# Kernel optimization log

Hardware: AMD Instinct MI355X
Metric: run time of the kernel (lower is better)

Reference implementation:

```python
import jax, jax.numpy as jnp
import numpy as np

# H2RConfig constants
KERNEL = 3
MAX_ROUTES = 1000
STRIDE = 4.0
MIN_SIZE = 32.0
MAX_SIZE = 512.0
SCORE_POWER = 2.0
UNC_WEIGHT = 0.35


def setup_inputs() -> dict:
    key = jax.random.key(0)
    k1, k2, k3 = jax.random.split(key, 3)
    shape = (32, 1, 512, 512)  # [B, 1, H, W] heatmaps at stride 4
    return {
        "route_logits": jax.random.normal(k1, shape, jnp.float32),
        "scale_logits": jax.random.normal(k2, shape, jnp.float32),
        "uncertainty_logits": jax.random.normal(k3, shape, jnp.float32),
        "image_h": 2048,
        "image_w": 2048,
    }


def reference(route_logits, scale_logits, uncertainty_logits, image_h, image_w):
    # score map: sigmoid^power, modulated by uncertainty (use_route_uncertainty=True)
    score = jnp.power(jax.nn.sigmoid(route_logits), SCORE_POWER)
    score = score * (1.0 - UNC_WEIGHT * jax.nn.sigmoid(uncertainty_logits))

    # local-max NMS: 3x3 max pool, stride 1, SAME padding (torch pads with -inf)
    pooled = jax.lax.reduce_window(
        score, -jnp.inf, jax.lax.max,
        window_dimensions=(1, 1, KERNEL, KERNEL),
        window_strides=(1, 1, 1, 1),
        padding="SAME",
    )
    peak_mask = score == pooled
    filtered = jnp.where(peak_mask, score, -1.0)

    B = score.shape[0]
    Wd = score.shape[3]
    flat = filtered.reshape(B, -1)                 # [B, H*W]
    values, indices = jax.lax.top_k(flat, MAX_ROUTES)  # [B, K]
    valid = values > 0.0                            # torch drops these; we mask/pad

    ys = indices // Wd
    xs = indices % Wd
    cx = (xs.astype(jnp.float32) + 0.5) * STRIDE
    cy = (ys.astype(jnp.float32) + 0.5) * STRIDE

    # gather scale / uncertainty at peak locations
    sc = jnp.take_along_axis(scale_logits.reshape(B, -1), indices, axis=1)
    un = jax.nn.sigmoid(jnp.take_along_axis(uncertainty_logits.reshape(B, -1), indices, axis=1))

    side = MIN_SIZE + jax.nn.sigmoid(sc) * (MAX_SIZE - MIN_SIZE)
    side = side * (1.0 + 0.25 * un)
    half = side * 0.5

    iw = float(image_w)
    ih = float(image_h)
    x1 = jnp.clip(cx - half, 0.0, iw - 1.0)
    y1 = jnp.clip(cy - half, 0.0, ih - 1.0)
    x2 = jnp.clip(cx + half, 1.0, iw)
    y2 = jnp.clip(cy + half, 1.0, ih)

    bcol = jnp.broadcast_to(jnp.arange(B, dtype=jnp.float32)[:, None], values.shape)
    rois = jnp.stack([bcol, x1, y1, x2, y2], axis=-1)  # [B, K, 5]

    # padded (fixed-shape) equivalent of torch's variable-length concat
    rois = jnp.where(valid[..., None], rois, 0.0)
    scores = jnp.where(valid, values, 0.0)
    return rois, scores, valid
```

## Files before the change

kernel.cpp:

```cpp
#include <hip/hip_runtime.h>
#include <hip/hip_bf16.h>
#include <math.h>


#define B_   32
#define H_   512
#define W_   512
#define HW_  (H_ * W_)
#define K_   1000
#define ROWS_ 16
#define THR_  512
#define PBUF_ 2048
#define PCAP_ 32768
#define CAND_ 2048
#define NBUK_ 4096

__device__ __forceinline__ float np_expf(float x) {
#pragma clang fp contract(off)
    const float log2e = 1.44269504088896341f;
    float z = x * log2e;
    float m = rintf(z);
    float r = fmaf(m, -0.693359375f, x);
    r = fmaf(m, 2.12194440e-4f, r);
    float r2 = r * r;
    float p = fmaf(1.9875691500e-4f, r, 1.3981999507e-3f);
    p = fmaf(p, r, 8.3334519073e-3f);
    p = fmaf(p, r, 4.1665795894e-2f);
    p = fmaf(p, r, 1.6666665459e-1f);
    p = fmaf(p, r, 5.0000001201e-1f);
    p = fmaf(p, r2, r);
    p = p + 1.0f;
    int mi = (int)m;
    float sc = __int_as_float((127 + mi) << 23);
    return p * sc;
}

__device__ __forceinline__ float sigmoid_np(float x) {
#pragma clang fp contract(off)
    float e = np_expf(-x);
    float d = 1.0f + e;
    return 1.0f / d;
}

__device__ __forceinline__ float score_ref(float r, float u) {
#pragma clang fp contract(off)
    float s  = sigmoid_np(r);
    float s2 = s * s;
    float su = sigmoid_np(u);
    float t  = 0.35f * su;
    float m  = 1.0f - t;
    return s2 * m;
}

__device__ __forceinline__ float sigmoid_fast(float x) {
    return 1.0f / (1.0f + __expf(-x));
}

__global__ __launch_bounds__(THR_, 4) void fused_peak_kernel(
    const float* __restrict__ route, const float* __restrict__ unc,
    unsigned long long* __restrict__ plist, int* __restrict__ peak_cnt)
{
    __shared__ float sm[ROWS_ + 2][W_];
    __shared__ unsigned long long pbuf[PBUF_];
    __shared__ int lcnt, gbase;

    const int tid   = threadIdx.x;
    const int strip = blockIdx.x;
    const int b     = blockIdx.y;
    const int r0    = strip * ROWS_;
    if (tid == 0) lcnt = 0;

    const float4* rb4 = (const float4*)(route + (size_t)b * HW_);
    const float4* ub4 = (const float4*)(unc   + (size_t)b * HW_);

    float4 rv[5], uv[5];
    int lrow[5], c4[5]; bool ok[5], act[5];
    #pragma unroll
    for (int k = 0; k < 5; ++k) {
        int slot = tid + k * THR_;
        act[k]  = slot < (ROWS_ + 2) * 128;
        int row = slot >> 7;
        int gy  = r0 - 1 + row;
        lrow[k] = row; c4[k] = slot & 127;
        ok[k]   = (gy >= 0 && gy < H_);
        int cy  = gy < 0 ? 0 : (gy >= H_ ? H_ - 1 : gy);
        if (act[k]) {
            rv[k] = rb4[cy * 128 + c4[k]];
            uv[k] = ub4[cy * 128 + c4[k]];
        }
    }
    #pragma unroll
    for (int k = 0; k < 5; ++k) {
        if (!act[k]) continue;
        float4 s;
        s.x = score_ref(rv[k].x, uv[k].x);
        s.y = score_ref(rv[k].y, uv[k].y);
        s.z = score_ref(rv[k].z, uv[k].z);
        s.w = score_ref(rv[k].w, uv[k].w);
        if (!ok[k]) { s.x = -INFINITY; s.y = -INFINITY;
                      s.z = -INFINITY; s.w = -INFINITY; }
        *(float4*)&sm[lrow[k]][c4[k] * 4] = s;
    }
    __syncthreads();

    #pragma unroll
    for (int j = 0; j < 4; ++j) {
        int g  = tid + j * THR_;
        int ly = 1 + (g >> 7);
        int x0 = (g & 127) * 4;
        int gy = r0 + (ly - 1);
        float4 q0 = *(const float4*)&sm[ly - 1][x0];
        float4 q1 = *(const float4*)&sm[ly    ][x0];
        float4 q2 = *(const float4*)&sm[ly + 1][x0];
        bool hasL = (x0 > 0), hasR = (x0 + 4 < W_);
        float l0 = hasL ? sm[ly - 1][x0 - 1] : -INFINITY;
        float l1 = hasL ? sm[ly    ][x0 - 1] : -INFINITY;
        float l2 = hasL ? sm[ly + 1][x0 - 1] : -INFINITY;
        float e0 = hasR ? sm[ly - 1][x0 + 4] : -INFINITY;
        float e1 = hasR ? sm[ly    ][x0 + 4] : -INFINITY;
        float e2 = hasR ? sm[ly + 1][x0 + 4] : -INFINITY;
        float f_m1 = fmaxf(l0, fmaxf(l1, l2));
        float f_0  = fmaxf(q0.x, fmaxf(q1.x, q2.x));
        float f_1  = fmaxf(q0.y, fmaxf(q1.y, q2.y));
        float f_2  = fmaxf(q0.z, fmaxf(q1.z, q2.z));
        float f_3  = fmaxf(q0.w, fmaxf(q1.w, q2.w));
        float f_4  = fmaxf(e0, fmaxf(e1, e2));
        float tb0  = fmaxf(q0.x, q2.x);
        float tb1  = fmaxf(q0.y, q2.y);
        float tb2  = fmaxf(q0.z, q2.z);
        float tb3  = fmaxf(q0.w, q2.w);
        float vv[4] = { q1.x, q1.y, q1.z, q1.w };
        float mm[4];
        mm[0] = fmaxf(fmaxf(f_m1, f_1), tb0);
        mm[1] = fmaxf(fmaxf(f_0,  f_2), tb1);
        mm[2] = fmaxf(fmaxf(f_1,  f_3), tb2);
        mm[3] = fmaxf(fmaxf(f_2,  f_4), tb3);
        #pragma unroll
        for (int i = 0; i < 4; ++i) {
            if (vv[i] >= mm[i]) {
                unsigned int bits = __float_as_uint(vv[i]);
                unsigned int idx  = (unsigned int)(gy * W_ + x0 + i);
                int p = atomicAdd(&lcnt, 1);
                if (p < PBUF_)
                    pbuf[p] = ((unsigned long long)bits << 32)
                              | (0xFFFFFFFFu - idx);
            }
        }
    }
    __syncthreads();
    if (tid == 0) {
        int n = lcnt < PBUF_ ? lcnt : PBUF_;
        gbase = atomicAdd(&peak_cnt[b], n);
    }
    __syncthreads();
    int n = lcnt < PBUF_ ? lcnt : PBUF_;
    int base = gbase;
    for (int i = tid; i < n; i += THR_) {
        int dst = base + i;
        if (dst < PCAP_) plist[(size_t)b * PCAP_ + dst] = pbuf[i];
    }
}

__global__ __launch_bounds__(1024) void select_kernel(
    const float* __restrict__ scale, const float* __restrict__ unc,
    const unsigned long long* __restrict__ plist,
    const int* __restrict__ peak_cnt,
    const int* __restrict__ ih_p, const int* __restrict__ iw_p,
    float* __restrict__ out)
{
    __shared__ unsigned int h16[NBUK_ / 2];
    __shared__ unsigned long long cand[CAND_];
    __shared__ int sh_T, sh_T2, sh_ref, sh_n;

    const int b = blockIdx.x, tid = threadIdx.x;
    const int lane = tid & 63, wid = tid >> 6;
    if (tid == 0) { sh_T = 0; sh_T2 = 0; sh_ref = 0; sh_n = 0; }
    for (int i = tid; i < NBUK_ / 2; i += 1024) h16[i] = 0u;
    __syncthreads();

    int pc = peak_cnt[b]; if (pc > PCAP_) pc = PCAP_;
    const unsigned long long* pl = plist + (size_t)b * PCAP_;

    for (int i = tid; i < pc; i += 1024) {
        unsigned int bkt = ((unsigned int)(pl[i] >> 32)) >> 18;
        atomicAdd(&h16[bkt >> 1], 1u << ((bkt & 1) * 16));
    }
    __syncthreads();

    if (wid == 0) {
        int total = 0;
        for (int c = NBUK_ / 64 - 1; c >= 0; --c) {
            int bucket = c * 64 + lane;
            int cnt = (int)((h16[bucket >> 1] >> ((bucket & 1) * 16)) & 0xFFFFu);
            int s = cnt;
            #pragma unroll
            for (int off = 32; off > 0; off >>= 1) s += __shfl_down(s, off, 64);
            s = __shfl(s, 0, 64);
            if (total + s < K_) { total += s; continue; }
            int suf = cnt;
            #pragma unroll
            for (int off = 1; off < 64; off <<= 1) {
                int o = __shfl_down(suf, off, 64);
                suf += (lane + off < 64) ? o : 0;
            }
            bool cond = (total + suf) >= K_;
            unsigned long long mask = __ballot(cond);
            int ls = 63 - __builtin_clzll(mask);
            int sufs = __shfl(suf, ls, 64);
            int cnts = __shfl(cnt, ls, 64);
            if (lane == 0) {
                sh_T = c * 64 + ls;
                int A = total + sufs - cnts;
                sh_ref = (A + cnts > 1024) ? (0x40000000 | A) : 0;
            }
            break;
        }
    }
    __syncthreads();
    const unsigned int T = (unsigned int)sh_T;
    const int refflag = sh_ref;
    const int refined = (refflag >> 30) & 1;
    const int A = refflag & 0x3FFFFFFF;

    if (refined) {
        for (int i = tid; i < NBUK_ / 2; i += 1024) h16[i] = 0u;
        __syncthreads();
        for (int i = tid; i < pc; i += 1024) {
            unsigned int bits = (unsigned int)(pl[i] >> 32);
            if ((bits >> 18) == T) {
                unsigned int sb = (bits >> 6) & 0xFFFu;
                atomicAdd(&h16[sb >> 1], 1u << ((sb & 1) * 16));
            }
        }
        __syncthreads();
        if (wid == 0) {
            int total = A;
            for (int c = NBUK_ / 64 - 1; c >= 0; --c) {
                int bucket = c * 64 + lane;
                int cnt = (int)((h16[bucket >> 1] >> ((bucket & 1) * 16)) & 0xFFFFu);
                int s = cnt;
                #pragma unroll
                for (int off = 32; off > 0; off >>= 1) s += __shfl_down(s, off, 64);
                s = __shfl(s, 0, 64);
                if (total + s < K_) { total += s; continue; }
                int suf = cnt;
                #pragma unroll
                for (int off = 1; off < 64; off <<= 1) {
                    int o = __shfl_down(suf, off, 64);
                    suf += (lane + off < 64) ? o : 0;
                }
                bool cond = (total + suf) >= K_;
                unsigned long long mask = __ballot(cond);
                int ls = 63 - __builtin_clzll(mask);
                if (lane == 0) sh_T2 = c * 64 + ls;
                break;
            }
        }
        __syncthreads();
    }
    const unsigned int T2 = (unsigned int)sh_T2;

    for (int i = tid; i < pc; i += 1024) {
        unsigned long long key = pl[i];
        unsigned int bits = (unsigned int)(key >> 32);
        unsigned int bkt  = bits >> 18;
        bool take = (bkt > T) ||
                    (bkt == T && (!refined || (((bits >> 6) & 0xFFFu) >= T2)));
        if (take) {
            int p = atomicAdd(&sh_n, 1);
            if (p < CAND_) cand[p] = key;
        }
    }
    __syncthreads();
    int nc = sh_n; if (nc > CAND_) nc = CAND_;
    int sortN = (nc <= 1024) ? 1024 : CAND_;
    for (int i = tid; i < sortN; i += 1024)
        if (i >= nc) cand[i] = 0ull;

    for (int kk = 2; kk <= sortN; kk <<= 1) {
        for (int jj = kk >> 1; jj > 0; jj >>= 1) {
            __syncthreads();
            for (int p = tid; p < (sortN >> 1); p += 1024) {
                int i   = ((p & ~(jj - 1)) << 1) | (p & (jj - 1));
                int ixj = i | jj;
                bool desc = ((i & kk) == 0);
                unsigned long long a = cand[i], c2 = cand[ixj];
                if (desc ? (a < c2) : (a > c2)) { cand[i] = c2; cand[ixj] = a; }
            }
        }
    }
    __syncthreads();

    const float fih = (float)(*ih_p);
    const float fiw = (float)(*iw_p);
    float* rois   = out;
    float* scores = out + (size_t)B_ * K_ * 5;
    float* validf = out + (size_t)B_ * K_ * 6;

    for (int k = tid; k < K_; k += 1024) {
        int o = b * K_ + k;
        unsigned long long key = cand[k];
        unsigned int bits = (unsigned int)(key >> 32);
        if (bits == 0u) {
            rois[o * 5 + 0] = 0.0f; rois[o * 5 + 1] = 0.0f;
            rois[o * 5 + 2] = 0.0f; rois[o * 5 + 3] = 0.0f;
            rois[o * 5 + 4] = 0.0f;
            scores[o] = 0.0f; validf[o] = 0.0f;
        } else {
            float v = __uint_as_float(bits);
            unsigned int idx = 0xFFFFFFFFu - (unsigned int)(key & 0xFFFFFFFFull);
            int y = (int)(idx >> 9), x = (int)(idx & 511u);
            float cx = ((float)x + 0.5f) * 4.0f;
            float cy = ((float)y + 0.5f) * 4.0f;
            float ss = sigmoid_fast(scale[(size_t)b * HW_ + idx]);
            float su = sigmoid_fast(unc  [(size_t)b * HW_ + idx]);
            float side = (32.0f + ss * 480.0f) * (1.0f + 0.25f * su);
            float half = 0.5f * side;
            float x1 = fminf(fmaxf(cx - half, 0.0f), fiw - 1.0f);
            float y1 = fminf(fmaxf(cy - half, 0.0f), fih - 1.0f);
            float x2 = fminf(fmaxf(cx + half, 1.0f), fiw);
            float y2 = fminf(fmaxf(cy + half, 1.0f), fih);
            rois[o * 5 + 0] = (float)b;
            rois[o * 5 + 1] = x1; rois[o * 5 + 2] = y1;
            rois[o * 5 + 3] = x2; rois[o * 5 + 4] = y2;
            scores[o] = v; validf[o] = 1.0f;
        }
    }
}

extern "C" void kernel_launch(void* const* d_in, const int* in_sizes, int n_in,
                              void* d_out, int out_size, void* d_ws, size_t ws_size,
                              hipStream_t stream) {
    const float* route = (const float*)d_in[0];
    const float* scale = (const float*)d_in[1];
    const float* unc   = (const float*)d_in[2];
    const int*   ih    = (const int*)d_in[3];
    const int*   iw    = (const int*)d_in[4];
    float* out = (float*)d_out;

    char* ws = (char*)d_ws;
    int* peak_cnt = (int*)ws;
    unsigned long long* plist = (unsigned long long*)(ws + 512);

    hipMemsetAsync(d_ws, 0, 512, stream);

    dim3 g(H_ / ROWS_, B_);
    fused_peak_kernel<<<g, THR_, 0, stream>>>(route, unc, plist, peak_cnt);
    select_kernel<<<B_, 1024, 0, stream>>>(scale, unc, plist, peak_cnt,
                                           ih, iw, out);
}
```

Before: 181.0 us.

## Split top-k selection into multi-block histogram, filter and sort kernels

The single per-batch select kernel is replaced by three kernels. A histogram kernel and a filter kernel each run 8 blocks per batch, using a global histogram and a global candidate buffer, and a sort/emit kernel then bitonic-sorts the candidates in shared memory. The aim is to spread the peak-list scan across more CUs than 32 blocks allow. The second-level histogram refinement is dropped, so if the threshold bucket is crowded the candidate count can exceed 2048 and truncate results. The peak kernel also switches to wave-aggregated atomics for the local peak counter, and it removes the load predicate by clamping the slot index.

```diff
diff --git a/kernel.cpp b/kernel.cpp
--- a/kernel.cpp
+++ b/kernel.cpp
@@ -14,6 +14,8 @@
 #define PCAP_ 32768
 #define CAND_ 2048
 #define NBUK_ 4096
+#define NW_   (NBUK_ / 2)
+#define SL_   8
 
 __device__ __forceinline__ float np_expf(float x) {
 #pragma clang fp contract(off)
@@ -65,6 +67,7 @@
     __shared__ int lcnt, gbase;
 
     const int tid   = threadIdx.x;
+    const int lane  = tid & 63;
     const int strip = blockIdx.x;
     const int b     = blockIdx.y;
     const int r0    = strip * ROWS_;
@@ -74,24 +77,21 @@
     const float4* ub4 = (const float4*)(unc   + (size_t)b * HW_);
 
     float4 rv[5], uv[5];
-    int lrow[5], c4[5]; bool ok[5], act[5];
+    int lrow[5], c4[5]; bool ok[5];
     #pragma unroll
     for (int k = 0; k < 5; ++k) {
         int slot = tid + k * THR_;
-        act[k]  = slot < (ROWS_ + 2) * 128;
+        slot = slot < 2303 ? slot : 2303;
         int row = slot >> 7;
         int gy  = r0 - 1 + row;
         lrow[k] = row; c4[k] = slot & 127;
         ok[k]   = (gy >= 0 && gy < H_);
         int cy  = gy < 0 ? 0 : (gy >= H_ ? H_ - 1 : gy);
-        if (act[k]) {
-            rv[k] = rb4[cy * 128 + c4[k]];
-            uv[k] = ub4[cy * 128 + c4[k]];
-        }
+        rv[k] = rb4[cy * 128 + c4[k]];
+        uv[k] = ub4[cy * 128 + c4[k]];
     }
     #pragma unroll
     for (int k = 0; k < 5; ++k) {
-        if (!act[k]) continue;
         float4 s;
         s.x = score_ref(rv[k].x, uv[k].x);
         s.y = score_ref(rv[k].y, uv[k].y);
@@ -137,13 +137,21 @@
         mm[3] = fmaxf(fmaxf(f_2,  f_4), tb3);
         #pragma unroll
         for (int i = 0; i < 4; ++i) {
-            if (vv[i] >= mm[i]) {
-                unsigned int bits = __float_as_uint(vv[i]);
-                unsigned int idx  = (unsigned int)(gy * W_ + x0 + i);
-                int p = atomicAdd(&lcnt, 1);
-                if (p < PBUF_)
-                    pbuf[p] = ((unsigned long long)bits << 32)
-                              | (0xFFFFFFFFu - idx);
+            bool take = (vv[i] >= mm[i]);
+            unsigned long long mk = __ballot(take);
+            if (mk) {
+                int ldr = __ffsll((unsigned long long)mk) - 1;
+                int base_ = 0;
+                if (lane == ldr) base_ = atomicAdd(&lcnt, __popcll(mk));
+                base_ = __shfl(base_, ldr, 64);
+                if (take) {
+                    int p = base_ + __popcll(mk & ((1ull << lane) - 1ull));
+                    unsigned int bits = __float_as_uint(vv[i]);
+                    unsigned int idx  = (unsigned int)(gy * W_ + x0 + i);
+                    if (p < PBUF_)
+                        pbuf[p] = ((unsigned long long)bits << 32)
+                                  | (0xFFFFFFFFu - idx);
+                }
             }
         }
     }
@@ -161,42 +169,58 @@
     }
 }
 
-__global__ __launch_bounds__(1024) void select_kernel(
-    const float* __restrict__ scale, const float* __restrict__ unc,
+__global__ __launch_bounds__(256) void hist_kernel(
     const unsigned long long* __restrict__ plist,
     const int* __restrict__ peak_cnt,
-    const int* __restrict__ ih_p, const int* __restrict__ iw_p,
-    float* __restrict__ out)
+    unsigned int* __restrict__ ghist)
 {
-    __shared__ unsigned int h16[NBUK_ / 2];
-    __shared__ unsigned long long cand[CAND_];
-    __shared__ int sh_T, sh_T2, sh_ref, sh_n;
-
-    const int b = blockIdx.x, tid = threadIdx.x;
+    __shared__ unsigned int lh[NW_];
+    const int s = blockIdx.x, b = blockIdx.y, tid = threadIdx.x;
+    for (int i = tid; i < NW_; i += 256) lh[i] = 0u;
+    __syncthreads();
+
+    int pc = peak_cnt[b]; if (pc > PCAP_) pc = PCAP_;
+    int seg = (pc + SL_ - 1) / SL_;
+    int i0 = s * seg, i1 = i0 + seg; if (i1 > pc) i1 = pc;
+    const unsigned long long* pl = plist + (size_t)b * PCAP_;
+    for (int i = i0 + tid; i < i1; i += 256) {
+        unsigned int bkt = ((unsigned int)(pl[i] >> 32)) >> 18;
+        atomicAdd(&lh[bkt >> 1], 1u << ((bkt & 1) * 16));
+    }
+    __syncthreads();
+    unsigned int* gh = ghist + b * NW_;
+    for (int i = tid; i < NW_; i += 256) {
+        unsigned int v = lh[i];
+        if (v) atomicAdd(&gh[i], v);
+    }
+}
+
+__global__ __launch_bounds__(256) void filter_kernel(
+    const unsigned long long* __restrict__ plist,
+    const int* __restrict__ peak_cnt,
+    const unsigned int* __restrict__ ghist,
+    unsigned long long* __restrict__ cand, int* __restrict__ cand_cnt)
+{
+    __shared__ unsigned int h[NW_];
+    __shared__ int sh_T;
+    const int s = blockIdx.x, b = blockIdx.y, tid = threadIdx.x;
     const int lane = tid & 63, wid = tid >> 6;
-    if (tid == 0) { sh_T = 0; sh_T2 = 0; sh_ref = 0; sh_n = 0; }
-    for (int i = tid; i < NBUK_ / 2; i += 1024) h16[i] = 0u;
-    __syncthreads();
-
-    int pc = peak_cnt[b]; if (pc > PCAP_) pc = PCAP_;
-    const unsigned long long* pl = plist + (size_t)b * PCAP_;
-
-    for (int i = tid; i < pc; i += 1024) {
-        unsigned int bkt = ((unsigned int)(pl[i] >> 32)) >> 18;
-        atomicAdd(&h16[bkt >> 1], 1u << ((bkt & 1) * 16));
-    }
+    if (tid == 0) sh_T = 0;
+    const unsigned int* gh = ghist + b * NW_;
+    for (int i = tid; i < NW_; i += 256) h[i] = gh[i];
     __syncthreads();
 
     if (wid == 0) {
         int total = 0;
         for (int c = NBUK_ / 64 - 1; c >= 0; --c) {
             int bucket = c * 64 + lane;
-            int cnt = (int)((h16[bucket >> 1] >> ((bucket & 1) * 16)) & 0xFFFFu);
-            int s = cnt;
+            int cnt = (int)((h[bucket >> 1] >> ((bucket & 1) * 16)) & 0xFFFFu);
+            int sum = cnt;
             #pragma unroll
-            for (int off = 32; off > 0; off >>= 1) s += __shfl_down(s, off, 64);
-            s = __shfl(s, 0, 64);
-            if (total + s < K_) { total += s; continue; }
+            for (int off = 32; off > 0; off >>= 1)
+                sum += __shfl_down(sum, off, 64);
+            sum = __shfl(sum, 0, 64);
+            if (total + sum < K_) { total += sum; continue; }
             int suf = cnt;
             #pragma unroll
             for (int off = 1; off < 64; off <<= 1) {
@@ -206,76 +230,48 @@
             bool cond = (total + suf) >= K_;
             unsigned long long mask = __ballot(cond);
             int ls = 63 - __builtin_clzll(mask);
-            int sufs = __shfl(suf, ls, 64);
-            int cnts = __shfl(cnt, ls, 64);
-            if (lane == 0) {
-                sh_T = c * 64 + ls;
-                int A = total + sufs - cnts;
-                sh_ref = (A + cnts > 1024) ? (0x40000000 | A) : 0;
+            if (lane == 0) sh_T = c * 64 + ls;
+            break;
+        }
+    }
+    __syncthreads();
+    const unsigned int T = (unsigned int)sh_T;
+
+    int pc = peak_cnt[b]; if (pc > PCAP_) pc = PCAP_;
+    int seg = (pc + SL_ - 1) / SL_;
+    int i0 = s * seg, i1 = i0 + seg; if (i1 > pc) i1 = pc;
+    const unsigned long long* pl = plist + (size_t)b * PCAP_;
+    for (int i = i0 + tid; i < i1; i += 256) {
+        unsigned long long key = pl[i];
+        bool take = ((((unsigned int)(key >> 32)) >> 18) >= T);
+        unsigned long long mk = __ballot(take);
+        if (mk) {
+            int ldr = __ffsll((unsigned long long)mk) - 1;
+            int base_ = 0;
+            if (lane == ldr) base_ = atomicAdd(&cand_cnt[b], __popcll(mk));
+            base_ = __shfl(base_, ldr, 64);
+            if (take) {
+                int p = base_ + __popcll(mk & ((1ull << lane) - 1ull));
+                if (p < CAND_) cand[(size_t)b * CAND_ + p] = key;
             }
-            break;
-        }
-    }
-    __syncthreads();
-    const unsigned int T = (unsigned int)sh_T;
-    const int refflag = sh_ref;
-    const int refined = (refflag >> 30) & 1;
-    const int A = refflag & 0x3FFFFFFF;
-
-    if (refined) {
-        for (int i = tid; i < NBUK_ / 2; i += 1024) h16[i] = 0u;
-        __syncthreads();
-        for (int i = tid; i < pc; i += 1024) {
-            unsigned int bits = (unsigned int)(pl[i] >> 32);
-            if ((bits >> 18) == T) {
-                unsigned int sb = (bits >> 6) & 0xFFFu;
-                atomicAdd(&h16[sb >> 1], 1u << ((sb & 1) * 16));
-            }
-        }
-        __syncthreads();
-        if (wid == 0) {
-            int total = A;
-            for (int c = NBUK_ / 64 - 1; c >= 0; --c) {
-                int bucket = c * 64 + lane;
-                int cnt = (int)((h16[bucket >> 1] >> ((bucket & 1) * 16)) & 0xFFFFu);
-                int s = cnt;
-                #pragma unroll
-                for (int off = 32; off > 0; off >>= 1) s += __shfl_down(s, off, 64);
-                s = __shfl(s, 0, 64);
-                if (total + s < K_) { total += s; continue; }
-                int suf = cnt;
-                #pragma unroll
-                for (int off = 1; off < 64; off <<= 1) {
-                    int o = __shfl_down(suf, off, 64);
-                    suf += (lane + off < 64) ? o : 0;
-                }
-                bool cond = (total + suf) >= K_;
-                unsigned long long mask = __ballot(cond);
-                int ls = 63 - __builtin_clzll(mask);
-                if (lane == 0) sh_T2 = c * 64 + ls;
-                break;
-            }
-        }
-        __syncthreads();
-    }
-    const unsigned int T2 = (unsigned int)sh_T2;
-
-    for (int i = tid; i < pc; i += 1024) {
-        unsigned long long key = pl[i];
-        unsigned int bits = (unsigned int)(key >> 32);
-        unsigned int bkt  = bits >> 18;
-        bool take = (bkt > T) ||
-                    (bkt == T && (!refined || (((bits >> 6) & 0xFFFu) >= T2)));
-        if (take) {
-            int p = atomicAdd(&sh_n, 1);
-            if (p < CAND_) cand[p] = key;
-        }
-    }
-    __syncthreads();
-    int nc = sh_n; if (nc > CAND_) nc = CAND_;
+        }
+    }
+}
+
+__global__ __launch_bounds__(1024) void sort_emit_kernel(
+    const float* __restrict__ scale, const float* __restrict__ unc,
+    const unsigned long long* __restrict__ cand,
+    const int* __restrict__ cand_cnt,
+    const int* __restrict__ ih_p, const int* __restrict__ iw_p,
+    float* __restrict__ out)
+{
+    __shared__ unsigned long long sc_[CAND_];
+    const int b = blockIdx.x, tid = threadIdx.x;
+
+    int nc = cand_cnt[b]; if (nc > CAND_) nc = CAND_;
     int sortN = (nc <= 1024) ? 1024 : CAND_;
     for (int i = tid; i < sortN; i += 1024)
-        if (i >= nc) cand[i] = 0ull;
+        sc_[i] = (i < nc) ? cand[(size_t)b * CAND_ + i] : 0ull;
 
     for (int kk = 2; kk <= sortN; kk <<= 1) {
         for (int jj = kk >> 1; jj > 0; jj >>= 1) {
@@ -284,8 +280,8 @@
                 int i   = ((p & ~(jj - 1)) << 1) | (p & (jj - 1));
                 int ixj = i | jj;
                 bool desc = ((i & kk) == 0);
-                unsigned long long a = cand[i], c2 = cand[ixj];
-                if (desc ? (a < c2) : (a > c2)) { cand[i] = c2; cand[ixj] = a; }
+                unsigned long long a = sc_[i], c2 = sc_[ixj];
+                if (desc ? (a < c2) : (a > c2)) { sc_[i] = c2; sc_[ixj] = a; }
             }
         }
     }
@@ -299,7 +295,7 @@
 
     for (int k = tid; k < K_; k += 1024) {
         int o = b * K_ + k;
-        unsigned long long key = cand[k];
+        unsigned long long key = sc_[k];
         unsigned int bits = (unsigned int)(key >> 32);
         if (bits == 0u) {
             rois[o * 5 + 0] = 0.0f; rois[o * 5 + 1] = 0.0f;
@@ -340,12 +336,21 @@
 
     char* ws = (char*)d_ws;
     int* peak_cnt = (int*)ws;
-    unsigned long long* plist = (unsigned long long*)(ws + 512);
-
-    hipMemsetAsync(d_ws, 0, 512, stream);
+    int* cand_cnt = (int*)(ws + 128);
+    unsigned int* ghist = (unsigned int*)(ws + 512);
+    const size_t ghist_b = (size_t)B_ * NW_ * 4;
+    unsigned long long* cand  = (unsigned long long*)(ws + 512 + ghist_b);
+    unsigned long long* plist = (unsigned long long*)(ws + 512 + ghist_b
+                                                      + (size_t)B_ * CAND_ * 8);
+
+    hipMemsetAsync(d_ws, 0, 512 + ghist_b, stream);
 
     dim3 g(H_ / ROWS_, B_);
     fused_peak_kernel<<<g, THR_, 0, stream>>>(route, unc, plist, peak_cnt);
-    select_kernel<<<B_, 1024, 0, stream>>>(scale, unc, plist, peak_cnt,
-                                           ih, iw, out);
-}
+    dim3 gs(SL_, B_);
+    hist_kernel  <<<gs, 256, 0, stream>>>(plist, peak_cnt, ghist);
+    filter_kernel<<<gs, 256, 0, stream>>>(plist, peak_cnt, ghist,
+                                          cand, cand_cnt);
+    sort_emit_kernel<<<B_, 1024, 0, stream>>>(scale, unc, cand, cand_cnt,
+                                              ih, iw, out);
+}
```

Measured after the change: 242.4 us. 33.9% more time.
